# Optimization experiments

Hardware: AMD Instinct MI355X
Metric: run time of the kernel (lower is better)

Reference implementation:

```python
import jax, jax.numpy as jnp
import numpy as np

B, S_MAX, E, H, D = 8, 4096, 4096, 32, 128
TOPK = 8
OFFSET = 4095  # decode position; cache has OFFSET prior tokens


def setup_inputs() -> dict:
    key = jax.random.key(0)
    ks = jax.random.split(key, 7)
    return {
        "x": jax.random.normal(ks[0], (B, 1, E), dtype=jnp.float32),
        "kv_cache": jax.random.normal(ks[1], (B, S_MAX, 2, H, D), dtype=jnp.float32),
        "w_qkv": jax.random.normal(ks[2], (3 * E, E), dtype=jnp.float32) * 0.02,
        "b_qkv": jax.random.normal(ks[3], (3 * E,), dtype=jnp.float32) * 0.02,
        "w_out": jax.random.normal(ks[4], (E, E), dtype=jnp.float32) * 0.02,
        "b_out": jax.random.normal(ks[5], (E,), dtype=jnp.float32) * 0.02,
        "batch_head_idx": jax.random.randint(ks[6], (B, TOPK), 0, H, dtype=jnp.int32),
        "seqlen_offset": OFFSET,
    }


def reference(x, kv_cache, w_qkv, b_qkv, w_out, b_out, batch_head_idx, seqlen_offset):
    batch = x.shape[0]
    # QKV projection: (B,1,3E) -> (B,1,3,H,D)
    qkv = (jnp.einsum("ble,fe->blf", x, w_qkv) + b_qkv).reshape(batch, 1, 3, H, D)
    q = qkv[:, :, 0]          # (B,1,H,D)
    kv_new = qkv[:, :, 1:]    # (B,1,2,H,D)

    # KV-cache scatter update at current position, then read prefix
    kv_cache = kv_cache.at[:, seqlen_offset:seqlen_offset + 1].set(kv_new)
    kv = kv_cache[:, : seqlen_offset + 1]  # (B,S,2,H,D)
    k = kv[:, :, 0]  # (B,S,H,D)
    v = kv[:, :, 1]  # (B,S,H,D)

    scale = 1.0 / jnp.sqrt(jnp.float32(D))
    # decode step: single query attends over full prefix (causal trivially satisfied)
    scores = jnp.einsum("bhd,bshd->bhs", q[:, 0], k) * scale  # (B,H,S)
    attn = jax.nn.softmax(scores, axis=-1)
    ctx = jnp.einsum("bhs,bshd->bhd", attn, v)  # (B,H,D)

    # select attention: only heads listed in batch_head_idx produce output
    sel = jnp.zeros((batch, H), dtype=ctx.dtype).at[
        jnp.arange(batch)[:, None], batch_head_idx
    ].set(1.0)
    ctx = ctx * sel[:, :, None]

    out = jnp.einsum("be,fe->bf", ctx.reshape(batch, E), w_out) + b_out
    return out.reshape(batch, 1, E)
```

## Files before the change

### kernel.cpp

```cpp
#include <hip/hip_runtime.h>
#include <cstdint>
#include <cmath>

#define B_    8
#define SMAX  4096
#define E_    4096
#define H_    32
#define D_    128
#define TOPK  8
#define NPAIR (B_*TOPK)
#define CHUNK 64
#define NCHUNK (SMAX/CHUNK)

#define WS_QKV  0
#define WS_M    (WS_QKV + NPAIR*384)
#define WS_L    (WS_M + NPAIR*NCHUNK)
#define WS_PCTX (WS_L + NPAIR*NCHUNK)
#define WS_CTX  (WS_PCTX + (size_t)NPAIR*NCHUNK*D_)

__global__ __launch_bounds__(256, 8) void k_qkv(const float* __restrict__ x,
    const float* __restrict__ w_qkv, const float* __restrict__ b_qkv,
    const int* __restrict__ bhi, float* __restrict__ ws)
{
    int gid = blockIdx.x;
    int h = gid / 384;
    int r = gid % 384;

    __shared__ int hs_s[B_*TOPK];
    __shared__ int nsel_s;
    __shared__ int sel_s[B_];
    __shared__ float part[4][B_];
    if (threadIdx.x < B_*TOPK) hs_s[threadIdx.x] = bhi[threadIdx.x];
    if (threadIdx.x == 0) nsel_s = 0;
    __syncthreads();
    if (threadIdx.x < B_) {
        int b = threadIdx.x;
        for (int j = 0; j < TOPK; ++j) {
            if (hs_s[b*TOPK + j] == h) {
                int idx = atomicAdd(&nsel_s, 1);
                sel_s[idx] = (b << 8) | j;
                break;
            }
        }
    }
    __syncthreads();
    int nsel = nsel_s;
    if (nsel == 0) return;

    int wid = threadIdx.x >> 6, lane = threadIdx.x & 63;
    int mat = r >> 7, rr = r & 127;
    int wrow = mat*E_ + h*D_ + rr;

    const float4* wp = (const float4*)(w_qkv + (size_t)wrow * E_) + wid*256;
    float4 wf[4];
    #pragma unroll
    for (int i = 0; i < 4; ++i) wf[i] = wp[i*64 + lane];

    for (int is = 0; is < nsel; ++is) {
        int b = sel_s[is] >> 8;
        const float4* xp = (const float4*)(x + (size_t)b * E_) + wid*256;
        float4 a = make_float4(0.f, 0.f, 0.f, 0.f);
        #pragma unroll
        for (int i = 0; i < 4; ++i) {
            float4 xv = xp[i*64 + lane];
            a.x += wf[i].x*xv.x; a.y += wf[i].y*xv.y;
            a.z += wf[i].z*xv.z; a.w += wf[i].w*xv.w;
        }
        float acc = (a.x + a.y) + (a.z + a.w);
        for (int o = 32; o > 0; o >>= 1) acc += __shfl_down(acc, o);
        if (lane == 0) part[wid][is] = acc;
    }
    __syncthreads();
    if (threadIdx.x < (unsigned)nsel) {
        int is = threadIdx.x;
        int b = sel_s[is] >> 8, slot = sel_s[is] & 255;
        int pair = b*TOPK + slot;
        float v = part[0][is] + part[1][is] + part[2][is] + part[3][is];
        ws[WS_QKV + pair*384 + r] = v + b_qkv[wrow];
    }
}

__global__ __launch_bounds__(256) void k_attn(const float* __restrict__ kv,
    const int* __restrict__ bhi, const int* __restrict__ seqoff,
    float* __restrict__ ws)
{
    int pair = blockIdx.x >> 6, chunk = blockIdx.x & (NCHUNK - 1);
    int b = pair >> 3, slot = pair & 7;
    int h = bhi[b*TOPK + slot];
    for (int j = 0; j < slot; ++j) if (bhi[b*TOPK + j] == h) return;
    int S = seqoff[0] + 1;

    __shared__ __align__(16) float4 q4_s[32];
    __shared__ float wts[CHUNK];
    __shared__ float red[8];
    __shared__ __align__(16) float4 vred[8][32];

    int tid = threadIdx.x;
    if (tid < 32) q4_s[tid] = ((const float4*)(ws + WS_QKV + pair*384))[tid];
    __syncthreads();

    int pos = tid >> 2, dq = tid & 3;
    int s = chunk*CHUNK + pos;
    bool valid = s < S;
    float sc = 0.f;
    if (valid) {
        const float4* kp = (s == S - 1)
            ? (const float4*)(ws + WS_QKV + pair*384 + 128)
            : (const float4*)(kv + ((((size_t)b*SMAX + s)*2 + 0)*H_ + h) * (size_t)D_);
        kp += dq*8;
        #pragma unroll
        for (int i = 0; i < 8; ++i) {
            float4 kvv = kp[i]; float4 qv = q4_s[dq*8 + i];
            sc += kvv.x*qv.x + kvv.y*qv.y + kvv.z*qv.z + kvv.w*qv.w;
        }
    }
    sc += __shfl_xor(sc, 1);
    sc += __shfl_xor(sc, 2);
    float score = valid ? sc * 0.08838834764831845f : -1e30f;

    float m = score;
    for (int o = 32; o > 0; o >>= 1) m = fmaxf(m, __shfl_down(m, o));
    int wid = tid >> 6, lane = tid & 63;
    if (lane == 0) red[wid] = m;
    __syncthreads();
    if (tid == 0) red[4] = fmaxf(fmaxf(red[0], red[1]), fmaxf(red[2], red[3]));
    __syncthreads();
    m = red[4];
    float w = (valid && dq == 0) ? expf(score - m) : 0.f;
    if (dq == 0) wts[pos] = w;
    float l = w;
    for (int o = 32; o > 0; o >>= 1) l += __shfl_down(l, o);
    if (lane == 0) red[wid] = l;
    __syncthreads();
    if (tid == 0) red[5] = red[0] + red[1] + red[2] + red[3];
    __syncthreads();

    int d4 = tid & 31, grp = tid >> 5;
    float4 acc = make_float4(0.f, 0.f, 0.f, 0.f);
    #pragma unroll
    for (int i = 0; i < 8; ++i) {
        int t = grp*8 + i;
        int s2 = chunk*CHUNK + t;
        if (s2 < S) {
            const float4* vp = (s2 == S - 1)
                ? (const float4*)(ws + WS_QKV + pair*384 + 256)
                : (const float4*)(kv + ((((size_t)b*SMAX + s2)*2 + 1)*H_ + h) * (size_t)D_);
            float4 vv = vp[d4];
            float wt = wts[t];
            acc.x += wt*vv.x; acc.y += wt*vv.y; acc.z += wt*vv.z; acc.w += wt*vv.w;
        }
    }
    vred[grp][d4] = acc;
    __syncthreads();

    int pc = pair*NCHUNK + chunk;
    if (tid < 32) {
        float4 r = vred[0][tid];
        #pragma unroll
        for (int g = 1; g < 8; ++g) {
            float4 o = vred[g][tid];
            r.x += o.x; r.y += o.y; r.z += o.z; r.w += o.w;
        }
        ((float4*)(ws + WS_PCTX + (size_t)pc*D_))[tid] = r;
    }
    if (tid == 0) { ws[WS_M + pc] = red[4]; ws[WS_L + pc] = red[5]; }
}

__global__ __launch_bounds__(128) void k_comb(const int* __restrict__ bhi,
    float* __restrict__ ws)
{
    int pair = blockIdx.x;
    int b = pair >> 3, slot = pair & 7;
    int tid = threadIdx.x;
    int h = bhi[b*TOPK + slot];
    bool dup = false;
    for (int j = 0; j < slot; ++j) if (bhi[b*TOPK + j] == h) dup = true;
    if (dup) { ws[WS_CTX + pair*D_ + tid] = 0.f; return; }

    __shared__ float m_s[NCHUNK], l_s[NCHUNK];
    if (tid < NCHUNK) {
        m_s[tid] = ws[WS_M + pair*NCHUNK + tid];
        l_s[tid] = ws[WS_L + pair*NCHUNK + tid];
    }
    __syncthreads();
    float M = -1e30f;
    for (int i = 0; i < NCHUNK; ++i) M = fmaxf(M, m_s[i]);
    float L = 0.f;
    for (int i = 0; i < NCHUNK; ++i) L += l_s[i] * expf(m_s[i] - M);
    float acc = 0.f;
    for (int i = 0; i < NCHUNK; ++i)
        acc += ws[WS_PCTX + (size_t)(pair*NCHUNK + i)*D_ + tid] * expf(m_s[i] - M);
    ws[WS_CTX + pair*D_ + tid] = acc / L;
}

__global__ __launch_bounds__(256) void k_out(const float* __restrict__ w_out,
    const float* __restrict__ b_out, const int* __restrict__ bhi,
    const float* __restrict__ ws, float* __restrict__ out)
{
    int b = blockIdx.x >> 7, fblk = blockIdx.x & 127;
    int tid = threadIdx.x;
    int f_local = tid >> 3, slot = tid & 7;
    int f = fblk*32 + f_local;

    __shared__ __align__(16) float ctx_s[TOPK*D_];
    __shared__ int h_s[TOPK];
    __shared__ int dup_s[TOPK];
    ((float4*)ctx_s)[tid] = ((const float4*)(ws + WS_CTX + (size_t)b*TOPK*D_))[tid];
    if (tid < TOPK) {
        int h = bhi[b*TOPK + tid]; h_s[tid] = h;
        int dup = 0;
        for (int j = 0; j < tid; ++j) if (bhi[b*TOPK + j] == h) dup = 1;
        dup_s[tid] = dup;
    }
    __syncthreads();

    float acc = 0.f;
    if (!dup_s[slot]) {
        const float4* wp = (const float4*)(w_out + (size_t)f*E_ + h_s[slot]*D_);
        const float4* cp = (const float4*)(ctx_s + slot*D_);
        #pragma unroll
        for (int i = 0; i < 32; ++i) {
            float4 wv = wp[i]; float4 cv = cp[i];
            acc += wv.x*cv.x + wv.y*cv.y + wv.z*cv.z + wv.w*cv.w;
        }
    }
    acc += __shfl_down(acc, 4, 8);
    acc += __shfl_down(acc, 2, 8);
    acc += __shfl_down(acc, 1, 8);
    if (slot == 0) out[(size_t)b*E_ + f] = acc + b_out[f];
}

extern "C" void kernel_launch(void* const* d_in, const int* in_sizes, int n_in,
                              void* d_out, int out_size, void* d_ws, size_t ws_size,
                              hipStream_t stream) {
    const float* x      = (const float*)d_in[0];
    const float* kv     = (const float*)d_in[1];
    const float* w_qkv  = (const float*)d_in[2];
    const float* b_qkv  = (const float*)d_in[3];
    const float* w_out  = (const float*)d_in[4];
    const float* b_out  = (const float*)d_in[5];
    const int*   bhi    = (const int*)d_in[6];
    const int*   seqoff = (const int*)d_in[7];
    float* ws  = (float*)d_ws;
    float* out = (float*)d_out;

    hipLaunchKernelGGL(k_qkv,  dim3(32*384),       dim3(256), 0, stream, x, w_qkv, b_qkv, bhi, ws);
    hipLaunchKernelGGL(k_attn, dim3(NPAIR*NCHUNK), dim3(256), 0, stream, kv, bhi, seqoff, ws);
    hipLaunchKernelGGL(k_comb, dim3(NPAIR),        dim3(128), 0, stream, bhi, ws);
    hipLaunchKernelGGL(k_out,  dim3(B_*128),       dim3(256), 0, stream, w_out, b_out, bhi, ws, out);
}
```

Baseline: 127.0 us.

## Restructure output projection per head to reuse w_out across batches with atomics

```diff
diff --git a/kernel.cpp b/kernel.cpp
--- a/kernel.cpp
+++ b/kernel.cpp
@@ -167,11 +167,21 @@
 }
 
 __global__ __launch_bounds__(128) void k_comb(const int* __restrict__ bhi,
-    float* __restrict__ ws)
+    const float* __restrict__ b_out, float* __restrict__ ws, float* __restrict__ out)
 {
     int pair = blockIdx.x;
     int b = pair >> 3, slot = pair & 7;
     int tid = threadIdx.x;
+
+    {
+        int bb = pair >> 3, fb = pair & 7;
+        #pragma unroll
+        for (int i = 0; i < 4; ++i) {
+            int f = fb*512 + i*128 + tid;
+            out[(size_t)bb*E_ + f] = b_out[f];
+        }
+    }
+
     int h = bhi[b*TOPK + slot];
     bool dup = false;
     for (int j = 0; j < slot; ++j) if (bhi[b*TOPK + j] == h) dup = true;
@@ -194,40 +204,61 @@
 }
 
 __global__ __launch_bounds__(256) void k_out(const float* __restrict__ w_out,
-    const float* __restrict__ b_out, const int* __restrict__ bhi,
-    const float* __restrict__ ws, float* __restrict__ out)
-{
-    int b = blockIdx.x >> 7, fblk = blockIdx.x & 127;
+    const int* __restrict__ bhi, const float* __restrict__ ws, float* __restrict__ out)
+{
+    int h = blockIdx.x >> 5, fblk = blockIdx.x & 31;
+
+    __shared__ int hs_s[B_*TOPK];
+    __shared__ int nsel_s;
+    __shared__ int sel_s[B_];
+    __shared__ __align__(16) float ctx_s[B_][D_];
     int tid = threadIdx.x;
-    int f_local = tid >> 3, slot = tid & 7;
-    int f = fblk*32 + f_local;
-
-    __shared__ __align__(16) float ctx_s[TOPK*D_];
-    __shared__ int h_s[TOPK];
-    __shared__ int dup_s[TOPK];
-    ((float4*)ctx_s)[tid] = ((const float4*)(ws + WS_CTX + (size_t)b*TOPK*D_))[tid];
-    if (tid < TOPK) {
-        int h = bhi[b*TOPK + tid]; h_s[tid] = h;
-        int dup = 0;
-        for (int j = 0; j < tid; ++j) if (bhi[b*TOPK + j] == h) dup = 1;
-        dup_s[tid] = dup;
-    }
-    __syncthreads();
-
-    float acc = 0.f;
-    if (!dup_s[slot]) {
-        const float4* wp = (const float4*)(w_out + (size_t)f*E_ + h_s[slot]*D_);
-        const float4* cp = (const float4*)(ctx_s + slot*D_);
-        #pragma unroll
-        for (int i = 0; i < 32; ++i) {
-            float4 wv = wp[i]; float4 cv = cp[i];
-            acc += wv.x*cv.x + wv.y*cv.y + wv.z*cv.z + wv.w*cv.w;
-        }
-    }
-    acc += __shfl_down(acc, 4, 8);
-    acc += __shfl_down(acc, 2, 8);
-    acc += __shfl_down(acc, 1, 8);
-    if (slot == 0) out[(size_t)b*E_ + f] = acc + b_out[f];
+    if (tid < B_*TOPK) hs_s[tid] = bhi[tid];
+    if (tid == 0) nsel_s = 0;
+    __syncthreads();
+    if (tid < B_) {
+        int b = tid;
+        for (int j = 0; j < TOPK; ++j) {
+            if (hs_s[b*TOPK + j] == h) {
+                int idx = atomicAdd(&nsel_s, 1);
+                sel_s[idx] = (b << 8) | j;
+                break;
+            }
+        }
+    }
+    __syncthreads();
+    int nsel = nsel_s;
+    if (nsel == 0) return;
+
+    for (int t = tid; t < nsel*32; t += 256) {
+        int is = t >> 5, q = t & 31;
+        int b = sel_s[is] >> 8, slot = sel_s[is] & 255;
+        ((float4*)ctx_s[is])[q] =
+            ((const float4*)(ws + WS_CTX + (size_t)(b*TOPK + slot)*D_))[q];
+    }
+    __syncthreads();
+
+    int f_local = tid >> 1, half = tid & 1;
+    int f = fblk*128 + f_local;
+    const float4* wp = (const float4*)(w_out + (size_t)f*E_ + h*D_) + half*16;
+    float4 wv[16];
+    #pragma unroll
+    for (int i = 0; i < 16; ++i) wv[i] = wp[i];
+
+    for (int is = 0; is < nsel; ++is) {
+        const float4* cp = (const float4*)ctx_s[is] + half*16;
+        float acc = 0.f;
+        #pragma unroll
+        for (int i = 0; i < 16; ++i) {
+            float4 c = cp[i];
+            acc += wv[i].x*c.x + wv[i].y*c.y + wv[i].z*c.z + wv[i].w*c.w;
+        }
+        acc += __shfl_xor(acc, 1);
+        if (half == 0) {
+            int b = sel_s[is] >> 8;
+            atomicAdd(&out[(size_t)b*E_ + f], acc);
+        }
+    }
 }
 
 extern "C" void kernel_launch(void* const* d_in, const int* in_sizes, int n_in,
@@ -246,6 +277,6 @@
 
     hipLaunchKernelGGL(k_qkv,  dim3(32*384),       dim3(256), 0, stream, x, w_qkv, b_qkv, bhi, ws);
     hipLaunchKernelGGL(k_attn, dim3(NPAIR*NCHUNK), dim3(256), 0, stream, kv, bhi, seqoff, ws);
-    hipLaunchKernelGGL(k_comb, dim3(NPAIR),        dim3(128), 0, stream, bhi, ws);
-    hipLaunchKernelGGL(k_out,  dim3(B_*128),       dim3(256), 0, stream, w_out, b_out, bhi, ws, out);
-}
+    hipLaunchKernelGGL(k_comb, dim3(NPAIR),        dim3(128), 0, stream, bhi, b_out, ws, out);
+    hipLaunchKernelGGL(k_out,  dim3(H_*32),        dim3(256), 0, stream, w_out, bhi, ws, out);
+}
```

New measurement: 117.2 us, median of 2. 7.8% less time.
